# Performance work log

Measured on AMD Instinct MI355X. Metric: run time of the kernel, lower is better.

## Reference

```python
import jax, jax.numpy as jnp
import numpy as np

B, N, H, W = 2, 2048, 256, 256
C = 128
STATE = 256
FEAT_IN = C + 2
MID = 6  # layer_num - 2 residual blocks
OUT_DIM = 2


def setup_inputs() -> dict:
    key = jax.random.key(0)
    ks = jax.random.split(key, 8)
    s = 0.01  # matches nn.Linear init normal_(0.0, 0.01)
    features = jax.random.normal(ks[0], (B, C, H, W), jnp.float32)
    base_point = jax.random.uniform(ks[1], (B, N, 2), dtype=jnp.float32)
    adj = jax.random.uniform(ks[2], (B, N, N), dtype=jnp.float32) / N  # row-normalized-ish adjacency
    point_mask = jnp.ones((B, 1, N, 1), jnp.float32)
    w_first = jax.random.normal(ks[3], (2, FEAT_IN, STATE), jnp.float32) * s  # fc1, fc2
    b_first = jnp.zeros((2, STATE), jnp.float32)
    w_mid = jax.random.normal(ks[4], (MID, 4, STATE, STATE), jnp.float32) * s  # per block: gcn1.fc1, gcn1.fc2, gcn2.fc1, gcn2.fc2
    b_mid = jnp.zeros((MID, 4, STATE), jnp.float32)
    w_last = jax.random.normal(ks[5], (2, STATE, STATE), jnp.float32) * s
    b_last = jnp.zeros((2, STATE), jnp.float32)
    w_fc = jax.random.normal(ks[6], (STATE, OUT_DIM), jnp.float32) * s
    b_fc = jnp.zeros((OUT_DIM,), jnp.float32)
    return dict(features=features, base_point=base_point, adj=adj, point_mask=point_mask,
                w_first=w_first, b_first=b_first, w_mid=w_mid, b_mid=b_mid,
                w_last=w_last, b_last=b_last, w_fc=w_fc, b_fc=b_fc)


def _interp(feat, coords, h, w):
    # feat: [B, H*W, C]; coords: [B, N, 2] in [0,1] (x, y order as in torch code)
    Xs = coords[:, :, 0] * w
    Ys = coords[:, :, 1] * h
    X0f = jnp.floor(Xs); X1f = X0f + 1.0
    Y0f = jnp.floor(Ys); Y1f = Y0f + 1.0
    w00 = (X1f - Xs) * (Y1f - Ys)
    w01 = (X1f - Xs) * (Ys - Y0f)
    w10 = (Xs - X0f) * (Y1f - Ys)
    w11 = (Xs - X0f) * (Ys - Y0f)
    X0 = jnp.clip(X0f, 0, w - 1).astype(jnp.int32)
    X1 = jnp.clip(X1f, 0, w - 1).astype(jnp.int32)
    Y0 = jnp.clip(Y0f, 0, h - 1).astype(jnp.int32)
    Y1 = jnp.clip(Y1f, 0, h - 1).astype(jnp.int32)
    def gather(idx):  # idx: [B, N] -> [B, N, C]
        return jnp.take_along_axis(feat, idx[:, :, None], axis=1)
    m00 = gather(X0 + Y0 * w)
    m01 = gather(X0 + Y1 * w)
    m10 = gather(X1 + Y0 * w)
    m11 = gather(X1 + Y1 * w)
    return (w00[..., None] * m00 + w01[..., None] * m01 +
            w10[..., None] * m10 + w11[..., None] * m11)


def _gconv(x, adj, w1, b1, w2, b2):
    # GraphConvolution: fc1(x) + fc2(adj @ x)
    return (x @ w1 + b1) + (jnp.matmul(adj, x) @ w2 + b2)


def _res_block(x, adj, w, b):
    h = jax.nn.relu(_gconv(x, adj, w[0], b[0], w[1], b[1]))
    h = _gconv(h, adj, w[2], b[2], w[3], b[3])
    return jax.nn.relu(h + x)


def _forward(features, base_point, adj, point_mask,
             w_first, b_first, w_mid, b_mid, w_last, b_last, w_fc, b_fc):
    b, c, h, w = features.shape
    feat_flat = features.reshape(b, c, h * w).transpose(0, 2, 1)  # [B, HW, C]
    cnn_feature = _interp(feat_flat, base_point, h, w)            # [B, N, C]
    x = jnp.concatenate([cnn_feature, base_point], axis=2)        # [B, N, C+2]
    x = _gconv(x, adj, w_first[0], b_first[0], w_first[1], b_first[1])
    for i in range(MID):
        x = _res_block(x, adj, w_mid[i], b_mid[i])
    x = _gconv(x, adj, w_last[0], b_last[0], w_last[1], b_last[1])
    gcn_pred = x @ w_fc + b_fc                                    # [B, N, out_dim]
    mask = point_mask.squeeze(1)                                  # [B, N, 1]
    pred_points = base_point + gcn_pred[:, :, :2] * mask
    lap1 = base_point - jnp.matmul(adj, base_point)
    lap2 = pred_points - jnp.matmul(adj, pred_points)
    lap_energy = jnp.sqrt((((lap2 - lap1) ** 2) + 1e-10).sum(-1)).mean(-1)  # [B]
    return pred_points, gcn_pred, lap_energy


def reference(features, base_point, adj, point_mask,
              w_first, b_first, w_mid, b_mid, w_last, b_last, w_fc, b_fc):
    return _forward(features, base_point, adj, point_mask,
                    w_first, b_first, w_mid, b_mid, w_last, b_last, w_fc, b_fc)
```

## Files before the change

kernel.cpp:

```cpp
#include <hip/hip_runtime.h>
#include <hip/hip_bf16.h>
#include <math.h>

#define BB 2
#define NN 2048
#define HH 256
#define WW 256
#define CC 128
#define MIDN 6
#define YSTR 1048576

typedef __hip_bfloat16 bf16;
typedef short short8 __attribute__((ext_vector_type(8)));
typedef float f32x4 __attribute__((ext_vector_type(4)));
typedef unsigned short ushort4v __attribute__((ext_vector_type(4)));

__device__ inline float bf2f(unsigned short u) {
    return __uint_as_float(((unsigned int)u) << 16);
}
__device__ inline unsigned short f2bf_bits(float f) {
    __hip_bfloat16 h = __float2bfloat16(f);
    return *reinterpret_cast<unsigned short*>(&h);
}

__global__ void prep_kernel(const float* __restrict__ adj, bf16* __restrict__ adjB,
                            const float* __restrict__ features, const float* __restrict__ base_point,
                            bf16* __restrict__ x0p,
                            const float* __restrict__ w_first, const float* __restrict__ w_mid,
                            const float* __restrict__ w_last, bf16* __restrict__ wT) {
    __shared__ float tbuf[32][33];
    int bid = blockIdx.x;
    int t = threadIdx.x;
    if (bid < 1024) {
        int wv = t >> 6, lane = t & 63;
        int idx = bid * 4 + wv;
        int b   = idx >> 11;
        float bx = base_point[idx * 2 + 0];
        float by = base_point[idx * 2 + 1];
        float xs = bx * (float)WW;
        float ys = by * (float)HH;
        float x0f = floorf(xs), y0f = floorf(ys);
        float x1f = x0f + 1.f, y1f = y0f + 1.f;
        float w00 = (x1f - xs) * (y1f - ys);
        float w01 = (x1f - xs) * (ys - y0f);
        float w10 = (xs - x0f) * (y1f - ys);
        float w11 = (xs - x0f) * (ys - y0f);
        int X0 = (int)fminf(fmaxf(x0f, 0.f), (float)(WW - 1));
        int X1 = (int)fminf(fmaxf(x1f, 0.f), (float)(WW - 1));
        int Y0 = (int)fminf(fmaxf(y0f, 0.f), (float)(HH - 1));
        int Y1 = (int)fminf(fmaxf(y1f, 0.f), (float)(HH - 1));
        int p00 = Y0 * WW + X0, p01 = Y1 * WW + X0;
        int p10 = Y0 * WW + X1, p11 = Y1 * WW + X1;
        int c0 = lane * 2;
        const float* f0 = features + (size_t)(b * CC + c0) * (HH * WW);
        const float* f1 = f0 + HH * WW;
        float v0 = w00 * f0[p00] + w01 * f0[p01] + w10 * f0[p10] + w11 * f0[p11];
        float v1 = w00 * f1[p00] + w01 * f1[p01] + w10 * f1[p10] + w11 * f1[p11];
        unsigned int pk = (unsigned int)f2bf_bits(v0) | ((unsigned int)f2bf_bits(v1) << 16);
        *(unsigned int*)(x0p + (size_t)idx * 256 + c0) = pk;
        unsigned int pk2 = 0;
        if (lane == 0)
            pk2 = (unsigned int)f2bf_bits(bx) | ((unsigned int)f2bf_bits(by) << 16);
        *(unsigned int*)(x0p + (size_t)idx * 256 + 128 + c0) = pk2;
    } else if (bid < 3072) {
        int sub = bid - 1024;
        size_t i = ((size_t)sub * 4096) + (size_t)t * 16;
        #pragma unroll
        for (int h = 0; h < 2; ++h) {
            float4 f0 = *(const float4*)(adj + i + h * 8);
            float4 f1 = *(const float4*)(adj + i + h * 8 + 4);
            short8 v;
            v[0] = (short)f2bf_bits(f0.x); v[1] = (short)f2bf_bits(f0.y);
            v[2] = (short)f2bf_bits(f0.z); v[3] = (short)f2bf_bits(f0.w);
            v[4] = (short)f2bf_bits(f1.x); v[5] = (short)f2bf_bits(f1.y);
            v[6] = (short)f2bf_bits(f1.z); v[7] = (short)f2bf_bits(f1.w);
            *(short8*)(adjB + i + h * 8) = v;
        }
    } else {
        int idx = bid - 3072;
        int m   = idx >> 6;
        int sub = idx & 63;
        int bx = sub & 7, by = sub >> 3;
        const float* S; int R;
        if (m < 2)       { S = w_first + (size_t)m * 130 * 256; R = 130; }
        else if (m < 26) { S = w_mid + (size_t)(m - 2) * 65536; R = 256; }
        else             { S = w_last + (size_t)(m - 26) * 65536; R = 256; }
        bf16* D = wT + (size_t)m * 65536;
        int tx = t & 31, ty = t >> 5;
        int c0 = bx * 32, r0 = by * 32;
        #pragma unroll
        for (int k = 0; k < 4; ++k) {
            int r = r0 + ty + 8 * k;
            tbuf[ty + 8 * k][tx] = (r < R) ? S[(size_t)r * 256 + c0 + tx] : 0.f;
        }
        __syncthreads();
        #pragma unroll
        for (int k = 0; k < 4; ++k) {
            int c = c0 + ty + 8 * k;
            D[(size_t)c * 256 + r0 + tx] = __float2bfloat16(tbuf[tx][ty + 8 * k]);
        }
    }
}

__global__ __launch_bounds__(256) void s_kernel(const bf16* __restrict__ gprev,
                                                const bf16* __restrict__ Yb,
                                                const float* __restrict__ bias1,
                                                const float* __restrict__ bias2,
                                                const bf16* __restrict__ res,
                                                int relu,
                                                const bf16* __restrict__ wcat,
                                                bf16* __restrict__ xR,
                                                bf16* __restrict__ g1out,
                                                bf16* __restrict__ g2T) {
    __shared__ bf16 Al[2 * 32 * 64];
    __shared__ bf16 Bl[2 * 128 * 64];
    int tid = threadIdx.x;
    int bid = blockIdx.x;
    int lin = (bid & 7) * 64 + (bid >> 3);
    int ct = lin & 3, rt = lin >> 2;
    int lane = tid & 63, w = tid >> 6;
    int wr = w >> 1, wc = w & 1;
    int row16 = lane & 15, kg = lane >> 4;

    int ad  = tid * 16;
    int arw = ad >> 7;
    int acb = ad & 127;
    int ridx = rt * 32 + arw;
    int awbyte = arw * 128 + (acb ^ ((arw & 7) << 4));
    int gc_base = acb >> 1;

    #define STAGE_B(buf, it)                                                              \
        _Pragma("unroll")                                                                 \
        for (int rnd = 0; rnd < 4; ++rnd) {                                               \
            int d = tid * 16 + rnd * 4096;                                                \
            int row = d >> 7;                                                             \
            int cb = d & 127;                                                             \
            int sc = (cb ^ ((row & 7) << 4)) >> 1;                                        \
            __builtin_amdgcn_global_load_lds(                                             \
                (const __attribute__((address_space(1))) void*)(wcat + (size_t)(ct * 128 + row) * 256 + (it) * 64 + sc), \
                (__attribute__((address_space(3))) void*)((char*)Bl + (buf) * 16384 + (w << 10) + rnd * 4096), \
                16, 0, 0);                                                                \
        }

    short8 gv, yv0, yv1, yv2, yv3, rv;
    #define LOADS_A(it)                                                                   \
        {                                                                                 \
            size_t off = (size_t)ridx * 256 + (it) * 64 + gc_base;                        \
            gv = *(const short8*)(gprev + off);                                           \
            if (Yb) {                                                                     \
                yv0 = *(const short8*)(Yb + off);                                         \
                yv1 = *(const short8*)(Yb + YSTR + off);                                  \
                yv2 = *(const short8*)(Yb + 2 * YSTR + off);                              \
                yv3 = *(const short8*)(Yb + 3 * YSTR + off);                              \
                if (res) rv = *(const short8*)(res + off);                                \
            }                                                                             \
        }

    #define COMBINE_WRITE_A(buf, it)                                                     \
        {                                                                                 \
            int gcol = (it) * 64 + gc_base;                                               \
            short8 pk;                                                                    \
            if (Yb) {                                                                     \
                _Pragma("unroll")                                                         \
                for (int j = 0; j < 8; ++j) {                                             \
                    float f = bf2f((unsigned short)gv[j]) + bf2f((unsigned short)yv0[j])  \
                            + bf2f((unsigned short)yv1[j]) + bf2f((unsigned short)yv2[j]) \
                            + bf2f((unsigned short)yv3[j])                                \
                            + bias1[gcol + j] + bias2[gcol + j];                          \
                    if (res)  f += bf2f((unsigned short)rv[j]);                           \
                    if (relu) f = fmaxf(f, 0.f);                                          \
                    pk[j] = (short)f2bf_bits(f);                                          \
                }                                                                         \
            } else {                                                                      \
                pk = gv;                                                                  \
            }                                                                             \
            if (ct == 0) *(short8*)(xR + (size_t)ridx * 256 + gcol) = pk;                 \
            *(short8*)((char*)Al + (buf) * 4096 + awbyte) = pk;                           \
        }

    f32x4 acc[4] = {};

    STAGE_B(0, 0);
    LOADS_A(0);
    COMBINE_WRITE_A(0, 0);
    asm volatile("s_waitcnt vmcnt(0) lgkmcnt(0)" ::: "memory");
    __builtin_amdgcn_s_barrier();

    #pragma unroll
    for (int it = 0; it < 4; ++it) {
        int cur = it & 1;
        if (it < 3) {
            STAGE_B(cur ^ 1, it + 1);
            LOADS_A(it + 1);
        }
        #pragma unroll
        for (int kk = 0; kk < 2; ++kk) {
            int arow = wr * 16 + row16;
            int abyte = cur * 4096 + arow * 128 + (((kk * 64) + kg * 16) ^ ((arow & 7) << 4));
            short8 a = *(const short8*)((const char*)Al + abyte);
            #pragma unroll
            for (int nf = 0; nf < 4; ++nf) {
                int fr = wc * 64 + nf * 16 + row16;
                int byte = cur * 16384 + fr * 128 + (((kk * 64) + kg * 16) ^ ((fr & 7) << 4));
                short8 bfr = *(const short8*)((const char*)Bl + byte);
                acc[nf] = __builtin_amdgcn_mfma_f32_16x16x32_bf16(a, bfr, acc[nf], 0, 0, 0);
            }
        }
        if (it < 3) {
            COMBINE_WRITE_A(cur ^ 1, it + 1);
            asm volatile("s_waitcnt vmcnt(0) lgkmcnt(0)" ::: "memory");
            __builtin_amdgcn_s_barrier();
        }
    }

    int cbase = ct * 128 + wc * 64;
    int rb = rt * 32 + wr * 16 + kg * 4;
    if (cbase < 256) {
        #pragma unroll
        for (int nf = 0; nf < 4; ++nf) {
            int c = cbase + nf * 16 + row16;
            #pragma unroll
            for (int j = 0; j < 4; ++j)
                *reinterpret_cast<unsigned short*>(&g1out[(size_t)(rb + j) * 256 + c]) = f2bf_bits(acc[nf][j]);
        }
    } else {
        #pragma unroll
        for (int nf = 0; nf < 4; ++nf) {
            int c = cbase - 256 + nf * 16 + row16;
            ushort4v pk;
            #pragma unroll
            for (int j = 0; j < 4; ++j) pk[j] = f2bf_bits(acc[nf][j]);
            *(ushort4v*)(g2T + (size_t)c * 4096 + rb) = pk;
        }
    }
    #undef STAGE_B
    #undef LOADS_A
    #undef COMBINE_WRITE_A
}

__global__ __launch_bounds__(256) void adjb_kernel(const bf16* __restrict__ adjB,
                                                   const bf16* __restrict__ g2T,
                                                   bf16* __restrict__ Ybase) {
    __shared__ bf16 Al[2 * 128 * 64];
    __shared__ bf16 Bl[2 * 64 * 64];
    int tid = threadIdx.x;
    int bid = blockIdx.x;
    int lin = (bid & 7) * 64 + (bid >> 3);
    int ct = lin & 3, rt = (lin >> 2) & 15, z = lin >> 6;
    int b = z >> 2, ks = z & 3;
    const bf16* Aadj = adjB + (size_t)b * NN * NN + (size_t)(rt * 128) * NN + ks * 512;
    const bf16* Bg   = g2T + (size_t)(ct * 64) * 4096 + b * NN + ks * 512;
    bf16* Yo = Ybase + (size_t)ks * YSTR;
    int lane = tid & 63, w = tid >> 6;
    int wr = w >> 1, wc = w & 1;
    int row16 = lane & 15, kg = lane >> 4;

    #define STAGE(buf, it)                                                                \
        {                                                                                 \
            int k0 = (it) * 64;                                                           \
            _Pragma("unroll")                                                             \
            for (int rnd = 0; rnd < 4; ++rnd) {                                           \
                int d = tid * 16 + rnd * 4096;                                            \
                int row = d >> 7, cb = d & 127;                                           \
                int sc = (cb ^ ((row & 7) << 4)) >> 1;                                    \
                __builtin_amdgcn_global_load_lds(                                         \
                    (const __attribute__((address_space(1))) void*)(Aadj + (size_t)row * NN + k0 + sc), \
                    (__attribute__((address_space(3))) void*)((char*)Al + (buf) * 16384 + (w << 10) + rnd * 4096), \
                    16, 0, 0);                                                            \
            }                                                                             \
            _Pragma("unroll")                                                             \
            for (int rnd = 0; rnd < 2; ++rnd) {                                           \
                int d = tid * 16 + rnd * 4096;                                            \
                int row = d >> 7, cb = d & 127;                                           \
                int sc = (cb ^ ((row & 7) << 4)) >> 1;                                    \
                __builtin_amdgcn_global_load_lds(                                         \
                    (const __attribute__((address_space(1))) void*)(Bg + (size_t)row * 4096 + k0 + sc), \
                    (__attribute__((address_space(3))) void*)((char*)Bl + (buf) * 8192 + (w << 10) + rnd * 4096), \
                    16, 0, 0);                                                            \
            }                                                                             \
        }

    f32x4 acc[4][2] = {};

    STAGE(0, 0);
    asm volatile("s_waitcnt vmcnt(0)" ::: "memory");
    __builtin_amdgcn_s_barrier();

    #pragma unroll 1
    for (int it = 0; it < 8; ++it) {
        int cur = it & 1;
        if (it < 7) STAGE(cur ^ 1, it + 1);
        #pragma unroll
        for (int kk = 0; kk < 2; ++kk) {
            short8 a[4], bfr[2];
            #pragma unroll
            for (int mf = 0; mf < 4; ++mf) {
                int row = wr * 64 + mf * 16 + row16;
                int byte = cur * 16384 + row * 128 + (((kk * 64) + kg * 16) ^ ((row & 7) << 4));
                a[mf] = *(const short8*)((const char*)Al + byte);
            }
            #pragma unroll
            for (int nf = 0; nf < 2; ++nf) {
                int fr = wc * 32 + nf * 16 + row16;
                int byte = cur * 8192 + fr * 128 + (((kk * 64) + kg * 16) ^ ((fr & 7) << 4));
                bfr[nf] = *(const short8*)((const char*)Bl + byte);
            }
            #pragma unroll
            for (int mf = 0; mf < 4; ++mf)
                #pragma unroll
                for (int nf = 0; nf < 2; ++nf)
                    acc[mf][nf] = __builtin_amdgcn_mfma_f32_16x16x32_bf16(a[mf], bfr[nf], acc[mf][nf], 0, 0, 0);
        }
        asm volatile("s_waitcnt vmcnt(0)" ::: "memory");
        __builtin_amdgcn_s_barrier();
    }

    #pragma unroll
    for (int mf = 0; mf < 4; ++mf) {
        #pragma unroll
        for (int nf = 0; nf < 2; ++nf) {
            int c  = ct * 64 + wc * 32 + nf * 16 + row16;
            int r0 = b * NN + rt * 128 + wr * 64 + mf * 16 + kg * 4;
            #pragma unroll
            for (int j = 0; j < 4; ++j)
                *reinterpret_cast<unsigned short*>(&Yo[(size_t)(r0 + j) * 256 + c]) = f2bf_bits(acc[mf][nf][j]);
        }
    }
    #undef STAGE
}

__global__ void head_kernel(const bf16* __restrict__ g1, const bf16* __restrict__ Yb,
                            const float* __restrict__ b_last,
                            const float* __restrict__ w_fc, const float* __restrict__ b_fc,
                            const float* __restrict__ base_point, const float* __restrict__ point_mask,
                            float* __restrict__ out, float* __restrict__ dpts) {
    int row = blockIdx.x * 256 + threadIdx.x;
    float s0 = b_fc[0], s1 = b_fc[1];
    for (int d = 0; d < 256; d += 8) {
        size_t off = (size_t)row * 256 + d;
        short8 a = *(const short8*)(g1 + off);
        float zv[8];
        #pragma unroll
        for (int j = 0; j < 8; ++j) zv[j] = bf2f((unsigned short)a[j]);
        #pragma unroll
        for (int p = 0; p < 4; ++p) {
            short8 yv = *(const short8*)(Yb + (size_t)p * YSTR + off);
            #pragma unroll
            for (int j = 0; j < 8; ++j) zv[j] += bf2f((unsigned short)yv[j]);
        }
        #pragma unroll
        for (int j = 0; j < 8; ++j) {
            float z = zv[j] + b_last[d + j] + b_last[256 + d + j];
            s0 += z * w_fc[(d + j) * 2 + 0];
            s1 += z * w_fc[(d + j) * 2 + 1];
        }
    }
    float m  = point_mask[row];
    float p0 = base_point[row * 2 + 0] + s0 * m;
    float p1 = base_point[row * 2 + 1] + s1 * m;
    out[row * 2 + 0] = p0;
    out[row * 2 + 1] = p1;
    out[2 * BB * NN + row * 2 + 0] = s0;
    out[2 * BB * NN + row * 2 + 1] = s1;
    dpts[row * 2 + 0] = s0 * m;
    dpts[row * 2 + 1] = s1 * m;
}

__global__ void lap_rows(const bf16* __restrict__ adjB, const float* __restrict__ dpts,
                         float* __restrict__ tvals) {
    int w    = threadIdx.x >> 6;
    int lane = threadIdx.x & 63;
    int row  = blockIdx.x * 4 + w;
    int b = row >> 11, n = row & 2047;
    const bf16* ar = adjB + (size_t)b * NN * NN + (size_t)n * NN;
    const float* db = dpts + (size_t)b * NN * 2;
    float s0 = 0.f, s1 = 0.f;
    for (int k4 = 0; k4 < 4; ++k4) {
        int k = k4 * 512 + lane * 8;
        short8 av = *(const short8*)(ar + k);
        #pragma unroll
        for (int j = 0; j < 8; ++j) {
            float a = bf2f((unsigned short)av[j]);
            float2 dv = *(const float2*)(db + (k + j) * 2);
            s0 += a * dv.x;
            s1 += a * dv.y;
        }
    }
    for (int off = 32; off; off >>= 1) {
        s0 += __shfl_xor(s0, off);
        s1 += __shfl_xor(s1, off);
    }
    if (lane == 0) {
        float e0 = dpts[(size_t)row * 2 + 0] - s0;
        float e1 = dpts[(size_t)row * 2 + 1] - s1;
        tvals[row] = sqrtf(e0 * e0 + e1 * e1 + 1e-10f);
    }
}

__global__ void lap_reduce(const float* __restrict__ tvals, float* __restrict__ outp) {
    __shared__ float sd[256];
    int b = blockIdx.x;
    float s = 0.f;
    for (int i = threadIdx.x; i < NN; i += 256) s += tvals[b * NN + i];
    sd[threadIdx.x] = s;
    __syncthreads();
    for (int o = 128; o; o >>= 1) {
        if (threadIdx.x < o) sd[threadIdx.x] += sd[threadIdx.x + o];
        __syncthreads();
    }
    if (threadIdx.x == 0) outp[b] = sd[0] / (float)NN;
}

extern "C" void kernel_launch(void* const* d_in, const int* in_sizes, int n_in,
                              void* d_out, int out_size, void* d_ws, size_t ws_size,
                              hipStream_t stream) {
    const float* features   = (const float*)d_in[0];
    const float* base_point = (const float*)d_in[1];
    const float* adj        = (const float*)d_in[2];
    const float* point_mask = (const float*)d_in[3];
    const float* w_first    = (const float*)d_in[4];
    const float* b_first    = (const float*)d_in[5];
    const float* w_mid      = (const float*)d_in[6];
    const float* b_mid      = (const float*)d_in[7];
    const float* w_last     = (const float*)d_in[8];
    const float* b_last     = (const float*)d_in[9];
    const float* w_fc       = (const float*)d_in[10];
    const float* b_fc       = (const float*)d_in[11];
    float* out = (float*)d_out;
    char* W = (char*)d_ws;

    bf16* adjB   = (bf16*)W;
    bf16* wT     = (bf16*)(W + 16777216);
    bf16* x0p    = (bf16*)(W + 20447232);
    bf16* g1b[2] = { (bf16*)(W + 22544384), (bf16*)(W + 24641536) };
    bf16* g2T    = (bf16*)(W + 26738688);
    bf16* Yb     = (bf16*)(W + 28835840);
    bf16* xsl[2] = { (bf16*)(W + 37224448), (bf16*)(W + 39321600) };
    bf16* xscr   = (bf16*)(W + 41418752);
    float* dpts  = (float*)(W + 43515904);
    float* tvals = (float*)(W + 43548672);

    prep_kernel<<<4864, 256, 0, stream>>>(adj, adjB, features, base_point, x0p,
                                          w_first, w_mid, w_last, wT);

    s_kernel<<<512, 256, 0, stream>>>(x0p, nullptr, nullptr, nullptr, nullptr, 0,
                                      wT, xscr, g1b[0], g2T);
    adjb_kernel<<<512, 256, 0, stream>>>(adjB, g2T, Yb);

    for (int k = 1; k < 14; ++k) {
        const float *bb1, *bb2;
        const bf16* resp = nullptr;
        bf16* xw;
        int rl;
        if (k == 1) {
            bb1 = b_first; bb2 = b_first + 256; rl = 0; xw = xsl[0];
        } else if ((k & 1) == 0) {
            int m = (k - 2) / 2;
            bb1 = b_mid + (size_t)m * 1024; bb2 = bb1 + 256;
            rl = 1; xw = xscr;
        } else {
            int m = (k - 3) / 2;
            bb1 = b_mid + (size_t)m * 1024 + 512; bb2 = bb1 + 256;
            rl = 1;
            resp = xsl[m & 1];
            xw   = xsl[((k - 1) / 2) & 1];
        }
        s_kernel<<<512, 256, 0, stream>>>(g1b[(k - 1) & 1], Yb, bb1, bb2, resp, rl,
                                          wT + (size_t)2 * k * 65536, xw, g1b[k & 1], g2T);
        adjb_kernel<<<512, 256, 0, stream>>>(adjB, g2T, Yb);
    }

    head_kernel<<<16, 256, 0, stream>>>(g1b[1], Yb, b_last, w_fc, b_fc,
                                        base_point, point_mask, out, dpts);
    lap_rows<<<1024, 256, 0, stream>>>(adjB, dpts, tvals);
    lap_reduce<<<BB, 256, 0, stream>>>(tvals, out + 4 * BB * NN);
}
```

Before: 333.1 us.

## Triple-buffer adjacency GEMM, single-shot s_kernel staging, fuse lap reduction via atomics

The adjacency GEMM kernel moves to a three-stage LDS ring with partial vmcnt waits, so two tiles of loads stay in flight while MFMAs run. s_kernel now stages the whole K=256 weight slab and A tile into LDS at once instead of double-buffering over four iterations, and both kernels get launch_bounds occupancy hints. The adj fp32-to-bf16 conversion uses half as many blocks, each doing twice the work. The lap_reduce kernel is replaced by per-block atomicAdd into the output, zeroed in head_kernel, which saves a launch but makes the float summation order nondeterministic.

Measured after the change: 324.6 us. -2.5%, faster.

```diff
diff --git a/kernel.cpp b/kernel.cpp
--- a/kernel.cpp
+++ b/kernel.cpp
@@ -62,11 +62,11 @@
         if (lane == 0)
             pk2 = (unsigned int)f2bf_bits(bx) | ((unsigned int)f2bf_bits(by) << 16);
         *(unsigned int*)(x0p + (size_t)idx * 256 + 128 + c0) = pk2;
-    } else if (bid < 3072) {
+    } else if (bid < 2048) {
         int sub = bid - 1024;
-        size_t i = ((size_t)sub * 4096) + (size_t)t * 16;
-        #pragma unroll
-        for (int h = 0; h < 2; ++h) {
+        size_t i = ((size_t)sub * 8192) + (size_t)t * 32;
+        #pragma unroll
+        for (int h = 0; h < 4; ++h) {
             float4 f0 = *(const float4*)(adj + i + h * 8);
             float4 f1 = *(const float4*)(adj + i + h * 8 + 4);
             short8 v;
@@ -77,7 +77,7 @@
             *(short8*)(adjB + i + h * 8) = v;
         }
     } else {
-        int idx = bid - 3072;
+        int idx = bid - 2048;
         int m   = idx >> 6;
         int sub = idx & 63;
         int bx = sub & 7, by = sub >> 3;
@@ -102,18 +102,19 @@
     }
 }
 
-__global__ __launch_bounds__(256) void s_kernel(const bf16* __restrict__ gprev,
-                                                const bf16* __restrict__ Yb,
-                                                const float* __restrict__ bias1,
-                                                const float* __restrict__ bias2,
-                                                const bf16* __restrict__ res,
-                                                int relu,
-                                                const bf16* __restrict__ wcat,
-                                                bf16* __restrict__ xR,
-                                                bf16* __restrict__ g1out,
-                                                bf16* __restrict__ g2T) {
-    __shared__ bf16 Al[2 * 32 * 64];
-    __shared__ bf16 Bl[2 * 128 * 64];
+__global__ __launch_bounds__(256, 2) void s_kernel(const bf16* __restrict__ gprev,
+                                                   const bf16* __restrict__ Yb,
+                                                   const float* __restrict__ bias1,
+                                                   const float* __restrict__ bias2,
+                                                   const bf16* __restrict__ res,
+                                                   int relu,
+                                                   const bf16* __restrict__ wcat,
+                                                   bf16* __restrict__ xR,
+                                                   bf16* __restrict__ g1out,
+                                                   bf16* __restrict__ g2T) {
+    __shared__ char lds[81920];
+    char* Bl = lds;
+    char* Al = lds + 65536;
     int tid = threadIdx.x;
     int bid = blockIdx.x;
     int lin = (bid & 7) * 64 + (bid >> 3);
@@ -122,94 +123,70 @@
     int wr = w >> 1, wc = w & 1;
     int row16 = lane & 15, kg = lane >> 4;
 
-    int ad  = tid * 16;
-    int arw = ad >> 7;
-    int acb = ad & 127;
-    int ridx = rt * 32 + arw;
-    int awbyte = arw * 128 + (acb ^ ((arw & 7) << 4));
-    int gc_base = acb >> 1;
-
-    #define STAGE_B(buf, it)                                                              \
-        _Pragma("unroll")                                                                 \
-        for (int rnd = 0; rnd < 4; ++rnd) {                                               \
-            int d = tid * 16 + rnd * 4096;                                                \
-            int row = d >> 7;                                                             \
-            int cb = d & 127;                                                             \
-            int sc = (cb ^ ((row & 7) << 4)) >> 1;                                        \
-            __builtin_amdgcn_global_load_lds(                                             \
-                (const __attribute__((address_space(1))) void*)(wcat + (size_t)(ct * 128 + row) * 256 + (it) * 64 + sc), \
-                (__attribute__((address_space(3))) void*)((char*)Bl + (buf) * 16384 + (w << 10) + rnd * 4096), \
-                16, 0, 0);                                                                \
-        }
-
-    short8 gv, yv0, yv1, yv2, yv3, rv;
-    #define LOADS_A(it)                                                                   \
-        {                                                                                 \
-            size_t off = (size_t)ridx * 256 + (it) * 64 + gc_base;                        \
-            gv = *(const short8*)(gprev + off);                                           \
-            if (Yb) {                                                                     \
-                yv0 = *(const short8*)(Yb + off);                                         \
-                yv1 = *(const short8*)(Yb + YSTR + off);                                  \
-                yv2 = *(const short8*)(Yb + 2 * YSTR + off);                              \
-                yv3 = *(const short8*)(Yb + 3 * YSTR + off);                              \
-                if (res) rv = *(const short8*)(res + off);                                \
-            }                                                                             \
-        }
-
-    #define COMBINE_WRITE_A(buf, it)                                                     \
-        {                                                                                 \
-            int gcol = (it) * 64 + gc_base;                                               \
-            short8 pk;                                                                    \
-            if (Yb) {                                                                     \
-                _Pragma("unroll")                                                         \
-                for (int j = 0; j < 8; ++j) {                                             \
-                    float f = bf2f((unsigned short)gv[j]) + bf2f((unsigned short)yv0[j])  \
-                            + bf2f((unsigned short)yv1[j]) + bf2f((unsigned short)yv2[j]) \
-                            + bf2f((unsigned short)yv3[j])                                \
-                            + bias1[gcol + j] + bias2[gcol + j];                          \
-                    if (res)  f += bf2f((unsigned short)rv[j]);                           \
-                    if (relu) f = fmaxf(f, 0.f);                                          \
-                    pk[j] = (short)f2bf_bits(f);                                          \
-                }                                                                         \
-            } else {                                                                      \
-                pk = gv;                                                                  \
-            }                                                                             \
-            if (ct == 0) *(short8*)(xR + (size_t)ridx * 256 + gcol) = pk;                 \
-            *(short8*)((char*)Al + (buf) * 4096 + awbyte) = pk;                           \
-        }
-
-    f32x4 acc[4] = {};
-
-    STAGE_B(0, 0);
-    LOADS_A(0);
-    COMBINE_WRITE_A(0, 0);
+    #pragma unroll
+    for (int rnd = 0; rnd < 16; ++rnd) {
+        int plane = rnd >> 2;
+        int dp = (rnd & 3) * 4096 + tid * 16;
+        int row = dp >> 7;
+        int cb = dp & 127;
+        int sc = (cb ^ ((row & 7) << 4)) >> 1;
+        __builtin_amdgcn_global_load_lds(
+            (const __attribute__((address_space(1))) void*)(wcat + (size_t)(ct * 128 + row) * 256 + plane * 64 + sc),
+            (__attribute__((address_space(3))) void*)(Bl + plane * 16384 + (rnd & 3) * 4096 + (w << 10)),
+            16, 0, 0);
+    }
+
+    {
+        int arow = tid >> 3;
+        int acb  = (tid * 16) & 127;
+        int ridx = rt * 32 + arow;
+        int awb  = arow * 128 + (acb ^ ((arow & 7) << 4));
+        #pragma unroll
+        for (int rnd = 0; rnd < 4; ++rnd) {
+            int gcol = rnd * 64 + (acb >> 1);
+            size_t off = (size_t)ridx * 256 + gcol;
+            short8 pk;
+            if (Yb) {
+                short8 gv  = *(const short8*)(gprev + off);
+                short8 y0v = *(const short8*)(Yb + off);
+                short8 y1v = *(const short8*)(Yb + YSTR + off);
+                short8 y2v = *(const short8*)(Yb + 2 * YSTR + off);
+                short8 y3v = *(const short8*)(Yb + 3 * YSTR + off);
+                short8 rv = {};
+                if (res) rv = *(const short8*)(res + off);
+                #pragma unroll
+                for (int j = 0; j < 8; ++j) {
+                    float f = bf2f((unsigned short)gv[j]) + bf2f((unsigned short)y0v[j])
+                            + bf2f((unsigned short)y1v[j]) + bf2f((unsigned short)y2v[j])
+                            + bf2f((unsigned short)y3v[j])
+                            + bias1[gcol + j] + bias2[gcol + j];
+                    if (res)  f += bf2f((unsigned short)rv[j]);
+                    if (relu) f = fmaxf(f, 0.f);
+                    pk[j] = (short)f2bf_bits(f);
+                }
+            } else {
+                pk = *(const short8*)(gprev + off);
+            }
+            if (ct == 0) *(short8*)(xR + off) = pk;
+            *(short8*)(Al + rnd * 4096 + awb) = pk;
+        }
+    }
+
     asm volatile("s_waitcnt vmcnt(0) lgkmcnt(0)" ::: "memory");
     __builtin_amdgcn_s_barrier();
 
+    f32x4 acc[4] = {};
+    int arow = wr * 16 + row16;
     #pragma unroll
-    for (int it = 0; it < 4; ++it) {
-        int cur = it & 1;
-        if (it < 3) {
-            STAGE_B(cur ^ 1, it + 1);
-            LOADS_A(it + 1);
-        }
-        #pragma unroll
-        for (int kk = 0; kk < 2; ++kk) {
-            int arow = wr * 16 + row16;
-            int abyte = cur * 4096 + arow * 128 + (((kk * 64) + kg * 16) ^ ((arow & 7) << 4));
-            short8 a = *(const short8*)((const char*)Al + abyte);
-            #pragma unroll
-            for (int nf = 0; nf < 4; ++nf) {
-                int fr = wc * 64 + nf * 16 + row16;
-                int byte = cur * 16384 + fr * 128 + (((kk * 64) + kg * 16) ^ ((fr & 7) << 4));
-                short8 bfr = *(const short8*)((const char*)Bl + byte);
-                acc[nf] = __builtin_amdgcn_mfma_f32_16x16x32_bf16(a, bfr, acc[nf], 0, 0, 0);
-            }
-        }
-        if (it < 3) {
-            COMBINE_WRITE_A(cur ^ 1, it + 1);
-            asm volatile("s_waitcnt vmcnt(0) lgkmcnt(0)" ::: "memory");
-            __builtin_amdgcn_s_barrier();
+    for (int kk = 0; kk < 8; ++kk) {
+        int plane = kk >> 1, kk2 = kk & 1;
+        int kof = kk2 * 64 + kg * 16;
+        short8 a = *(const short8*)(Al + plane * 4096 + arow * 128 + (kof ^ ((arow & 7) << 4)));
+        #pragma unroll
+        for (int nf = 0; nf < 4; ++nf) {
+            int fr = wc * 64 + nf * 16 + row16;
+            short8 bfr = *(const short8*)(Bl + plane * 16384 + fr * 128 + (kof ^ ((fr & 7) << 4)));
+            acc[nf] = __builtin_amdgcn_mfma_f32_16x16x32_bf16(a, bfr, acc[nf], 0, 0, 0);
         }
     }
 
@@ -233,16 +210,12 @@
             *(ushort4v*)(g2T + (size_t)c * 4096 + rb) = pk;
         }
     }
-    #undef STAGE_B
-    #undef LOADS_A
-    #undef COMBINE_WRITE_A
-}
-
-__global__ __launch_bounds__(256) void adjb_kernel(const bf16* __restrict__ adjB,
-                                                   const bf16* __restrict__ g2T,
-                                                   bf16* __restrict__ Ybase) {
-    __shared__ bf16 Al[2 * 128 * 64];
-    __shared__ bf16 Bl[2 * 64 * 64];
+}
+
+__global__ __launch_bounds__(256, 2) void adjb_kernel(const bf16* __restrict__ adjB,
+                                                      const bf16* __restrict__ g2T,
+                                                      bf16* __restrict__ Ybase) {
+    __shared__ char lds[73728];
     int tid = threadIdx.x;
     int bid = blockIdx.x;
     int lin = (bid & 7) * 64 + (bid >> 3);
@@ -254,10 +227,11 @@
     int lane = tid & 63, w = tid >> 6;
     int wr = w >> 1, wc = w & 1;
     int row16 = lane & 15, kg = lane >> 4;
-
-    #define STAGE(buf, it)                                                                \
+    f32x4 acc[4][2] = {};
+
+    #define STAGE(BUF, IT)                                                                \
         {                                                                                 \
-            int k0 = (it) * 64;                                                           \
+            int k0 = (IT) * 64;                                                           \
             _Pragma("unroll")                                                             \
             for (int rnd = 0; rnd < 4; ++rnd) {                                           \
                 int d = tid * 16 + rnd * 4096;                                            \
@@ -265,7 +239,7 @@
                 int sc = (cb ^ ((row & 7) << 4)) >> 1;                                    \
                 __builtin_amdgcn_global_load_lds(                                         \
                     (const __attribute__((address_space(1))) void*)(Aadj + (size_t)row * NN + k0 + sc), \
-                    (__attribute__((address_space(3))) void*)((char*)Al + (buf) * 16384 + (w << 10) + rnd * 4096), \
+                    (__attribute__((address_space(3))) void*)(lds + (BUF) * 24576 + rnd * 4096 + (w << 10)), \
                     16, 0, 0);                                                            \
             }                                                                             \
             _Pragma("unroll")                                                             \
@@ -275,45 +249,51 @@
                 int sc = (cb ^ ((row & 7) << 4)) >> 1;                                    \
                 __builtin_amdgcn_global_load_lds(                                         \
                     (const __attribute__((address_space(1))) void*)(Bg + (size_t)row * 4096 + k0 + sc), \
-                    (__attribute__((address_space(3))) void*)((char*)Bl + (buf) * 8192 + (w << 10) + rnd * 4096), \
+                    (__attribute__((address_space(3))) void*)(lds + (BUF) * 24576 + 16384 + rnd * 4096 + (w << 10)), \
                     16, 0, 0);                                                            \
             }                                                                             \
         }
 
-    f32x4 acc[4][2] = {};
+    #define MFMA_STEP(BUF)                                                                \
+        _Pragma("unroll")                                                                 \
+        for (int kk = 0; kk < 2; ++kk) {                                                  \
+            short8 a[4], bfr[2];                                                          \
+            _Pragma("unroll")                                                             \
+            for (int mf = 0; mf < 4; ++mf) {                                              \
+                int row = wr * 64 + mf * 16 + row16;                                      \
+                a[mf] = *(const short8*)(lds + (BUF) * 24576 + row * 128 +                \
+                          (((kk * 64) + kg * 16) ^ ((row & 7) << 4)));                    \
+            }                                                                             \
+            _Pragma("unroll")                                                             \
+            for (int nf = 0; nf < 2; ++nf) {                                              \
+                int fr = wc * 32 + nf * 16 + row16;                                       \
+                bfr[nf] = *(const short8*)(lds + (BUF) * 24576 + 16384 + fr * 128 +       \
+                          (((kk * 64) + kg * 16) ^ ((fr & 7) << 4)));                     \
+            }                                                                             \
+            _Pragma("unroll")                                                             \
+            for (int mf = 0; mf < 4; ++mf)                                                \
+                _Pragma("unroll")                                                         \
+                for (int nf = 0; nf < 2; ++nf)                                            \
+                    acc[mf][nf] = __builtin_amdgcn_mfma_f32_16x16x32_bf16(a[mf], bfr[nf], acc[mf][nf], 0, 0, 0); \
+        }
+
+    #define ADJB_ITER(BUF, SBUF, DOSTAGE, CNT)                                            \
+        if (DOSTAGE) { STAGE(SBUF, SIT); }                                                \
+        asm volatile("s_waitcnt vmcnt(" #CNT ")" ::: "memory");                           \
+        __builtin_amdgcn_s_barrier();                                                     \
+        MFMA_STEP(BUF);                                                                   \
+        __builtin_amdgcn_s_barrier();
 
     STAGE(0, 0);
-    asm volatile("s_waitcnt vmcnt(0)" ::: "memory");
-    __builtin_amdgcn_s_barrier();
-
-    #pragma unroll 1
-    for (int it = 0; it < 8; ++it) {
-        int cur = it & 1;
-        if (it < 7) STAGE(cur ^ 1, it + 1);
-        #pragma unroll
-        for (int kk = 0; kk < 2; ++kk) {
-            short8 a[4], bfr[2];
-            #pragma unroll
-            for (int mf = 0; mf < 4; ++mf) {
-                int row = wr * 64 + mf * 16 + row16;
-                int byte = cur * 16384 + row * 128 + (((kk * 64) + kg * 16) ^ ((row & 7) << 4));
-                a[mf] = *(const short8*)((const char*)Al + byte);
-            }
-            #pragma unroll
-            for (int nf = 0; nf < 2; ++nf) {
-                int fr = wc * 32 + nf * 16 + row16;
-                int byte = cur * 8192 + fr * 128 + (((kk * 64) + kg * 16) ^ ((fr & 7) << 4));
-                bfr[nf] = *(const short8*)((const char*)Bl + byte);
-            }
-            #pragma unroll
-            for (int mf = 0; mf < 4; ++mf)
-                #pragma unroll
-                for (int nf = 0; nf < 2; ++nf)
-                    acc[mf][nf] = __builtin_amdgcn_mfma_f32_16x16x32_bf16(a[mf], bfr[nf], acc[mf][nf], 0, 0, 0);
-        }
-        asm volatile("s_waitcnt vmcnt(0)" ::: "memory");
-        __builtin_amdgcn_s_barrier();
-    }
+    STAGE(1, 1);
+    { enum { SIT = 2 }; ADJB_ITER(0, 2, 1, 12) }
+    { enum { SIT = 3 }; ADJB_ITER(1, 0, 1, 12) }
+    { enum { SIT = 4 }; ADJB_ITER(2, 1, 1, 12) }
+    { enum { SIT = 5 }; ADJB_ITER(0, 2, 1, 12) }
+    { enum { SIT = 6 }; ADJB_ITER(1, 0, 1, 12) }
+    { enum { SIT = 7 }; ADJB_ITER(2, 1, 1, 12) }
+    { enum { SIT = 0 }; ADJB_ITER(0, 0, 0, 6) }
+    { enum { SIT = 0 }; ADJB_ITER(1, 0, 0, 0) }
 
     #pragma unroll
     for (int mf = 0; mf < 4; ++mf) {
@@ -327,6 +307,8 @@
         }
     }
     #undef STAGE
+    #undef MFMA_STEP
+    #undef ADJB_ITER
 }
 
 __global__ void head_kernel(const bf16* __restrict__ g1, const bf16* __restrict__ Yb,
@@ -334,6 +316,8 @@
                             const float* __restrict__ w_fc, const float* __restrict__ b_fc,
                             const float* __restrict__ base_point, const float* __restrict__ point_mask,
                             float* __restrict__ out, float* __restrict__ dpts) {
+    if (blockIdx.x == 0 && threadIdx.x < 2)
+        out[4 * BB * NN + threadIdx.x] = 0.f;
     int row = blockIdx.x * 256 + threadIdx.x;
     float s0 = b_fc[0], s1 = b_fc[1];
     for (int d = 0; d < 256; d += 8) {
@@ -367,7 +351,8 @@
 }
 
 __global__ void lap_rows(const bf16* __restrict__ adjB, const float* __restrict__ dpts,
-                         float* __restrict__ tvals) {
+                         float* __restrict__ outlap) {
+    __shared__ float sd[4];
     int w    = threadIdx.x >> 6;
     int lane = threadIdx.x & 63;
     int row  = blockIdx.x * 4 + w;
@@ -393,22 +378,13 @@
     if (lane == 0) {
         float e0 = dpts[(size_t)row * 2 + 0] - s0;
         float e1 = dpts[(size_t)row * 2 + 1] - s1;
-        tvals[row] = sqrtf(e0 * e0 + e1 * e1 + 1e-10f);
-    }
-}
-
-__global__ void lap_reduce(const float* __restrict__ tvals, float* __restrict__ outp) {
-    __shared__ float sd[256];
-    int b = blockIdx.x;
-    float s = 0.f;
-    for (int i = threadIdx.x; i < NN; i += 256) s += tvals[b * NN + i];
-    sd[threadIdx.x] = s;
+        sd[w] = sqrtf(e0 * e0 + e1 * e1 + 1e-10f);
+    }
     __syncthreads();
-    for (int o = 128; o; o >>= 1) {
-        if (threadIdx.x < o) sd[threadIdx.x] += sd[threadIdx.x + o];
-        __syncthreads();
-    }
-    if (threadIdx.x == 0) outp[b] = sd[0] / (float)NN;
+    if (threadIdx.x == 0) {
+        float s = (sd[0] + sd[1] + sd[2] + sd[3]) * (1.f / (float)NN);
+        atomicAdd(&outlap[b], s);
+    }
 }
 
 extern "C" void kernel_launch(void* const* d_in, const int* in_sizes, int n_in,
@@ -438,9 +414,8 @@
     bf16* xsl[2] = { (bf16*)(W + 37224448), (bf16*)(W + 39321600) };
     bf16* xscr   = (bf16*)(W + 41418752);
     float* dpts  = (float*)(W + 43515904);
-    float* tvals = (float*)(W + 43548672);
-
-    prep_kernel<<<4864, 256, 0, stream>>>(adj, adjB, features, base_point, x0p,
+
+    prep_kernel<<<3840, 256, 0, stream>>>(adj, adjB, features, base_point, x0p,
                                           w_first, w_mid, w_last, wT);
 
     s_kernel<<<512, 256, 0, stream>>>(x0p, nullptr, nullptr, nullptr, nullptr, 0,
@@ -472,6 +447,5 @@
 
     head_kernel<<<16, 256, 0, stream>>>(g1b[1], Yb, b_last, w_fc, b_fc,
                                         base_point, point_mask, out, dpts);
-    lap_rows<<<1024, 256, 0, stream>>>(adjB, dpts, tvals);
-    lap_reduce<<<BB, 256, 0, stream>>>(tvals, out + 4 * BB * NN);
-}
+    lap_rows<<<1024, 256, 0, stream>>>(adjB, dpts, out + 4 * BB * NN);
+}
```
